# Optimization experiments

Measured on AMD Instinct MI355X. Metric: run time of the kernel, lower is better.

The kernel has to match this reference:

```python
import jax, jax.numpy as jnp
import numpy as np

EMBED_DIM = 1024
NUM_HEADS = 16
HEAD_DIM = EMBED_DIM // NUM_HEADS
LN_EPS = 1e-12
B, S = 2, 2048


def setup_inputs() -> dict:
    key = jax.random.key(0)
    ks = jax.random.split(key, 12)
    scale = 1.0 / np.sqrt(EMBED_DIM)
    d = EMBED_DIM
    return {
        "in_features": jax.random.normal(ks[0], (B, S, d), dtype=jnp.float32),
        "tgt_mask": jnp.ones((B, S), dtype=jnp.float32),
        "Wq": jax.random.normal(ks[1], (d, d), dtype=jnp.float32) * scale,
        "bq": jnp.zeros((d,), dtype=jnp.float32),
        "Wk": jax.random.normal(ks[2], (d, d), dtype=jnp.float32) * scale,
        "bk": jnp.zeros((d,), dtype=jnp.float32),
        "Wv": jax.random.normal(ks[3], (d, d), dtype=jnp.float32) * scale,
        "bv": jnp.zeros((d,), dtype=jnp.float32),
        "Wo": jax.random.normal(ks[4], (d, d), dtype=jnp.float32) * scale,
        "bo": jnp.zeros((d,), dtype=jnp.float32),
        "gamma": jnp.ones((d,), dtype=jnp.float32),
        "beta": jnp.zeros((d,), dtype=jnp.float32),
    }


def _split_heads(x):  # [B,S,D] -> [B,H,S,Dh]
    b, s, _ = x.shape
    return x.reshape(b, s, NUM_HEADS, HEAD_DIM).transpose(0, 2, 1, 3)


def reference(in_features, tgt_mask, Wq, bq, Wk, bk, Wv, bv, Wo, bo, gamma, beta):
    # Self-attention (tgt_features defaults to in_features). Dropout in eval mode (identity).
    q = _split_heads(in_features @ Wq.T + bq)
    k = _split_heads(in_features @ Wk.T + bk)
    v = _split_heads(in_features @ Wv.T + bv)
    # scores: [B,H,S,S]
    scores = jnp.einsum("bhqd,bhkd->bhqk", q, k) / jnp.sqrt(jnp.float32(HEAD_DIM))
    scores = scores + (1.0 - tgt_mask)[:, None, None, :] * (-100000.0)
    attn = jax.nn.softmax(scores, axis=-1)
    ctx = jnp.einsum("bhqk,bhkd->bhqd", attn, v)  # [B,H,S,Dh]
    ctx = ctx.transpose(0, 2, 1, 3).reshape(in_features.shape)  # merge heads
    out = ctx @ Wo.T + bo
    x = out + in_features
    mu = jnp.mean(x, axis=-1, keepdims=True)
    var = jnp.mean(jnp.square(x - mu), axis=-1, keepdims=True)
    return (x - mu) / jnp.sqrt(var + LN_EPS) * gamma + beta
```

## Files before the change

kernel.cpp:

```cpp
#include <hip/hip_runtime.h>
#include <hip/hip_bf16.h>

#define DM   1024
#define HEADS 16
#define DH    64
#define SEQ  2048
#define BATCH   2

typedef __attribute__((ext_vector_type(8))) short short8;
typedef __attribute__((ext_vector_type(4))) short bf16x4;
typedef __attribute__((ext_vector_type(4))) float floatx4;

__device__ __forceinline__ short f2b(float f) {
    union { float f; unsigned u; } v; v.f = f;
    unsigned r = v.u + 0x7FFFu + ((v.u >> 16) & 1u);
    return (short)(r >> 16);
}

__device__ __forceinline__ void async_copy16(const short* gsrc, short* ldst) {
    __builtin_amdgcn_global_load_lds(
        (const __attribute__((address_space(1))) void*)gsrc,
        (__attribute__((address_space(3))) void*)ldst,
        16, 0, 0);
}

__global__ __launch_bounds__(256) void cvt_all(const float* __restrict__ x,
        const float* __restrict__ wq, const float* __restrict__ wk,
        const float* __restrict__ wv, const float* __restrict__ wo,
        short* __restrict__ xb, short* __restrict__ wqkv, short* __restrict__ wob)
{
    const int b = blockIdx.x;
    const float* src; short* dst; int idx;
    if (b < 4096)      { src = x;  dst = xb;                idx = b; }
    else if (b < 5120) { src = wq; dst = wqkv;              idx = b - 4096; }
    else if (b < 6144) { src = wk; dst = wqkv + (1 << 20);  idx = b - 5120; }
    else if (b < 7168) { src = wv; dst = wqkv + (2 << 20);  idx = b - 6144; }
    else               { src = wo; dst = wob;               idx = b - 7168; }
    const int i = idx * 256 + threadIdx.x;
    floatx4 v = ((const floatx4*)src)[i];
    bf16x4 o;
    o.x = f2b(v.x); o.y = f2b(v.y); o.z = f2b(v.z); o.w = f2b(v.w);
    ((bf16x4*)dst)[i] = o;
}

__global__ __launch_bounds__(256) void gemm_qkv(const short* __restrict__ A,
        const short* __restrict__ B,
        const float* __restrict__ bq, const float* __restrict__ bk,
        const float* __restrict__ bv,
        short* __restrict__ qw, short* __restrict__ kw, short* __restrict__ vw)
{
    __shared__ short As[128 * 32];
    __shared__ short Bs[128 * 32];
    const int m0 = blockIdx.x * 128, n0 = blockIdx.y * 128;
    const int w = threadIdx.x >> 6, lane = threadIdx.x & 63;
    const int l16 = lane & 15, quad = lane >> 4;
    const int wm = w >> 1, wn = w & 1;
    const int lr = lane >> 2, lc = (lane & 3) * 8;

    floatx4 acc[4][4];
#pragma unroll
    for (int i = 0; i < 4; ++i)
#pragma unroll
        for (int j = 0; j < 4; ++j) acc[i][j] = (floatx4){0.f, 0.f, 0.f, 0.f};

    for (int kt = 0; kt < DM / 32; ++kt) {
        const int k0 = kt * 32;
        __syncthreads();
        async_copy16(A + (size_t)(m0 + w * 32 + lr) * DM + k0 + lc,      &As[w * 1024]);
        async_copy16(A + (size_t)(m0 + w * 32 + 16 + lr) * DM + k0 + lc, &As[w * 1024 + 512]);
        async_copy16(B + (size_t)(n0 + w * 32 + lr) * DM + k0 + lc,      &Bs[w * 1024]);
        async_copy16(B + (size_t)(n0 + w * 32 + 16 + lr) * DM + k0 + lc, &Bs[w * 1024 + 512]);
        __syncthreads();

        short8 af[4], bf[4];
#pragma unroll
        for (int i = 0; i < 4; ++i)
            af[i] = *(const short8*)&As[(wm * 64 + i * 16 + l16) * 32 + quad * 8];
#pragma unroll
        for (int j = 0; j < 4; ++j)
            bf[j] = *(const short8*)&Bs[(wn * 64 + j * 16 + l16) * 32 + quad * 8];
#pragma unroll
        for (int i = 0; i < 4; ++i)
#pragma unroll
            for (int j = 0; j < 4; ++j)
                acc[i][j] = __builtin_amdgcn_mfma_f32_16x16x32_bf16(af[i], bf[j], acc[i][j], 0, 0, 0);
    }

    const int m_base = m0 + wm * 64 + quad * 4;
#pragma unroll
    for (int j = 0; j < 4; ++j) {
        const int nb = n0 + wn * 64 + j * 16;
        const int t = nb >> 10;
        const int nn = (nb & 1023) + l16;
        const int h = nn >> 6, dh = nn & 63;
        const float* bias = (t == 0) ? bq : (t == 1) ? bk : bv;
        short* dst = (t == 0) ? qw : (t == 1) ? kw : vw;
        const float mulf = (t == 0) ? 0.125f : 1.0f;
        const float bvv = bias[nn];
#pragma unroll
        for (int i = 0; i < 4; ++i)
#pragma unroll
            for (int r = 0; r < 4; ++r) {
                const int m = m_base + i * 16 + r;
                const int b = m >> 11, s = m & (SEQ - 1);
                dst[(((size_t)(b * HEADS + h)) * SEQ + s) * DH + dh] =
                    f2b((acc[i][j][r] + bvv) * mulf);
            }
    }
}

__global__ __launch_bounds__(256) void transpose_v(const short* __restrict__ v,
                                                   short* __restrict__ vt)
{
    __shared__ short tl[64][72];
    const int st = blockIdx.x;
    const int bh = blockIdx.y;
    const int t = threadIdx.x;
    const int row = t >> 2, off = (t & 3) * 16;
    const short* vp = v + ((size_t)bh * SEQ + st * 64 + row) * DH + off;
    *(short8*)&tl[row][off]     = *(const short8*)vp;
    *(short8*)&tl[row][off + 8] = *(const short8*)(vp + 8);
    __syncthreads();
    short8 o0, o1;
#pragma unroll
    for (int j = 0; j < 8; ++j) { o0[j] = tl[off + j][row]; o1[j] = tl[off + 8 + j][row]; }
    short* op = vt + ((size_t)bh * DH + row) * SEQ + st * 64 + off;
    *(short8*)op = o0;
    *(short8*)(op + 8) = o1;
}

__global__ __launch_bounds__(256) void attn_kernel(const short* __restrict__ q,
        const short* __restrict__ k, const short* __restrict__ vt,
        const float* __restrict__ mask, short* __restrict__ ctx)
{
    const int qtile = blockIdx.x;
    const int bh    = blockIdx.y;
    const int bidx  = bh >> 4;
    const int wave = threadIdx.x >> 6, lane = threadIdx.x & 63;
    const int l16 = lane & 15, quad = lane >> 4;
    const int lx = l16 & 7;

    __shared__ short k_lds[64 * 64];
    __shared__ short v_lds[64 * 64];
    __shared__ short p_lds[4][16 * 64];
    __shared__ float madd_lds[SEQ];

    {
        const int t = threadIdx.x;
        const float* mrow = mask + (size_t)bidx * SEQ;
#pragma unroll
        for (int i = 0; i < 8; ++i) {
            const int idx = t * 8 + i;
            madd_lds[idx] = (1.f - mrow[idx]) * (-100000.f);
        }
    }

    const int qrow = qtile * 64 + wave * 16 + l16;
    const short* qbase = q + ((size_t)bh * SEQ + qrow) * DH;
    short8 b_q[2];
#pragma unroll
    for (int ks = 0; ks < 2; ++ks)
        b_q[ks] = *(const short8*)(qbase + ks * 32 + quad * 8);

    float m_own = -1e30f;
    floatx4 o[4];
    floatx4 l_acc = (floatx4){0.f, 0.f, 0.f, 0.f};
#pragma unroll
    for (int d = 0; d < 4; ++d) o[d] = (floatx4){0.f, 0.f, 0.f, 0.f};

    short8 ones;
#pragma unroll
    for (int j = 0; j < 8; ++j) ones[j] = (short)0x3F80;

    const short* kbase0 = k  + (size_t)bh * SEQ * DH;
    const short* vbase0 = vt + (size_t)bh * DH * SEQ;

    for (int kt = 0; kt < SEQ / 64; ++kt) {
        __syncthreads();
        {
            const short* kbase = kbase0 + (size_t)(kt * 64) * DH;
            const short* vbase = vbase0 + kt * 64;
#pragma unroll
            for (int i = 0; i < 2; ++i) {
                const int slot = i * 256 + wave * 64 + lane;
                const int row = slot >> 3, c = slot & 7;
                const int g = c ^ (row & 7);
                async_copy16(kbase + row * DH  + g * 8, &k_lds[(i * 256 + wave * 64) * 8]);
                async_copy16(vbase + (size_t)row * SEQ + g * 8, &v_lds[(i * 256 + wave * 64) * 8]);
            }
        }
        __syncthreads();

        float sv[4][4];
#pragma unroll
        for (int nt = 0; nt < 4; ++nt) {
            floatx4 acc = *(const floatx4*)&madd_lds[kt * 64 + nt * 16 + quad * 4];
#pragma unroll
            for (int ks = 0; ks < 2; ++ks) {
                short8 a = *(const short8*)
                    &k_lds[(nt * 16 + l16) * 64 + (((ks * 4 + quad) ^ lx) * 8)];
                acc = __builtin_amdgcn_mfma_f32_16x16x32_bf16(a, b_q[ks], acc, 0, 0, 0);
            }
#pragma unroll
            for (int r = 0; r < 4; ++r) sv[nt][r] = acc[r];
        }

        float tm = sv[0][0];
#pragma unroll
        for (int nt = 0; nt < 4; ++nt)
#pragma unroll
            for (int r = 0; r < 4; ++r) tm = fmaxf(tm, sv[nt][r]);
        tm = fmaxf(tm, __shfl_xor(tm, 16));
        tm = fmaxf(tm, __shfl_xor(tm, 32));
        const int upd = __any(tm > m_own);
        const float nm = fmaxf(m_own, tm);

#pragma unroll
        for (int nt = 0; nt < 4; ++nt) {
            const float p0 = __expf(sv[nt][0] - nm);
            const float p1 = __expf(sv[nt][1] - nm);
            const float p2 = __expf(sv[nt][2] - nm);
            const float p3 = __expf(sv[nt][3] - nm);
            union { __hip_bfloat162 h[2]; bf16x4 v; } u;
            u.h[0] = __float22bfloat162_rn(make_float2(p0, p1));
            u.h[1] = __float22bfloat162_rn(make_float2(p2, p3));
            *(bf16x4*)&p_lds[wave][l16 * 64 +
                (((nt * 2 + (quad >> 1)) ^ lx) * 8) + (quad & 1) * 4] = u.v;
        }

        if (upd) {
            const float alpha = __expf(m_own - nm);
            float ab[4];
#pragma unroll
            for (int r = 0; r < 4; ++r)
                ab[r] = __shfl(alpha, (lane & 48) | (quad * 4 + r));
#pragma unroll
            for (int d = 0; d < 4; ++d)
#pragma unroll
                for (int r = 0; r < 4; ++r) o[d][r] *= ab[r];
#pragma unroll
            for (int r = 0; r < 4; ++r) l_acc[r] *= ab[r];
        }
        m_own = nm;

#pragma unroll
        for (int ks2 = 0; ks2 < 2; ++ks2) {
            short8 pf = *(const short8*)
                &p_lds[wave][l16 * 64 + (((ks2 * 4 + quad) ^ lx) * 8)];
#pragma unroll
            for (int d = 0; d < 4; ++d) {
                short8 vf = *(const short8*)
                    &v_lds[(d * 16 + l16) * 64 + (((ks2 * 4 + quad) ^ lx) * 8)];
                o[d] = __builtin_amdgcn_mfma_f32_16x16x32_bf16(pf, vf, o[d], 0, 0, 0);
            }
            l_acc = __builtin_amdgcn_mfma_f32_16x16x32_bf16(pf, ones, l_acc, 0, 0, 0);
        }
    }

    const int h = bh & 15, bb = bh >> 4;
    const int srow = qtile * 64 + wave * 16 + quad * 4;
    float rl[4];
#pragma unroll
    for (int r = 0; r < 4; ++r) rl[r] = 1.f / l_acc[r];
#pragma unroll
    for (int d = 0; d < 4; ++d) {
        const int dh = d * 16 + l16;
#pragma unroll
        for (int r = 0; r < 4; ++r) {
            const float val = o[d][r] * rl[r];
            ctx[((size_t)(bb * SEQ + srow + r)) * DM + h * 64 + dh] = f2b(val);
        }
    }
}

__global__ __launch_bounds__(256) void gemm_o(const short* __restrict__ A,
        const short* __restrict__ B, const float* __restrict__ bo,
        const float* __restrict__ xin, float* __restrict__ out)
{
    __shared__ short As[128 * 32];
    __shared__ short Bs[128 * 32];
    const int m0 = blockIdx.x * 128, n0 = blockIdx.y * 128;
    const int w = threadIdx.x >> 6, lane = threadIdx.x & 63;
    const int l16 = lane & 15, quad = lane >> 4;
    const int wm = w >> 1, wn = w & 1;
    const int lr = lane >> 2, lc = (lane & 3) * 8;

    floatx4 acc[4][4];
#pragma unroll
    for (int i = 0; i < 4; ++i)
#pragma unroll
        for (int j = 0; j < 4; ++j) acc[i][j] = (floatx4){0.f, 0.f, 0.f, 0.f};

    for (int kt = 0; kt < DM / 32; ++kt) {
        const int k0 = kt * 32;
        __syncthreads();
        async_copy16(A + (size_t)(m0 + w * 32 + lr) * DM + k0 + lc,      &As[w * 1024]);
        async_copy16(A + (size_t)(m0 + w * 32 + 16 + lr) * DM + k0 + lc, &As[w * 1024 + 512]);
        async_copy16(B + (size_t)(n0 + w * 32 + lr) * DM + k0 + lc,      &Bs[w * 1024]);
        async_copy16(B + (size_t)(n0 + w * 32 + 16 + lr) * DM + k0 + lc, &Bs[w * 1024 + 512]);
        __syncthreads();

        short8 af[4], bf[4];
#pragma unroll
        for (int i = 0; i < 4; ++i)
            af[i] = *(const short8*)&As[(wm * 64 + i * 16 + l16) * 32 + quad * 8];
#pragma unroll
        for (int j = 0; j < 4; ++j)
            bf[j] = *(const short8*)&Bs[(wn * 64 + j * 16 + l16) * 32 + quad * 8];
#pragma unroll
        for (int i = 0; i < 4; ++i)
#pragma unroll
            for (int j = 0; j < 4; ++j)
                acc[i][j] = __builtin_amdgcn_mfma_f32_16x16x32_bf16(af[i], bf[j], acc[i][j], 0, 0, 0);
    }

    const int m_base = m0 + wm * 64 + quad * 4;
#pragma unroll
    for (int j = 0; j < 4; ++j) {
        const int n = n0 + wn * 64 + j * 16 + l16;
        const float bvv = bo[n];
#pragma unroll
        for (int i = 0; i < 4; ++i)
#pragma unroll
            for (int r = 0; r < 4; ++r) {
                const int m = m_base + i * 16 + r;
                const size_t idx = (size_t)m * DM + n;
                out[idx] = acc[i][j][r] + bvv + xin[idx];
            }
    }
}

__global__ __launch_bounds__(256) void ln_kernel(float* __restrict__ y,
        const float* __restrict__ gamma, const float* __restrict__ beta)
{
    const int row = blockIdx.x;
    const int t = threadIdx.x;
    const int wave = t >> 6, lane = t & 63;
    const floatx4 v = ((const floatx4*)(y + (size_t)row * DM))[t];
    float s  = v.x + v.y + v.z + v.w;
    float q2 = v.x * v.x + v.y * v.y + v.z * v.z + v.w * v.w;
#pragma unroll
    for (int off = 1; off < 64; off <<= 1) {
        s  += __shfl_xor(s, off);
        q2 += __shfl_xor(q2, off);
    }
    __shared__ float rs[4], rq[4];
    if (lane == 0) { rs[wave] = s; rq[wave] = q2; }
    __syncthreads();
    const float S  = rs[0] + rs[1] + rs[2] + rs[3];
    const float Q2 = rq[0] + rq[1] + rq[2] + rq[3];
    const float mu = S * (1.f / DM);
    float var = Q2 * (1.f / DM) - mu * mu;
    var = fmaxf(var, 0.f);
    const float rstd = rsqrtf(var + 1e-12f);
    const floatx4 g = ((const floatx4*)gamma)[t];
    const floatx4 bt = ((const floatx4*)beta)[t];
    floatx4 o;
    o.x = (v.x - mu) * rstd * g.x + bt.x;
    o.y = (v.y - mu) * rstd * g.y + bt.y;
    o.z = (v.z - mu) * rstd * g.z + bt.z;
    o.w = (v.w - mu) * rstd * g.w + bt.w;
    ((floatx4*)(y + (size_t)row * DM))[t] = o;
}

extern "C" void kernel_launch(void* const* d_in, const int* in_sizes, int n_in,
                              void* d_out, int out_size, void* d_ws, size_t ws_size,
                              hipStream_t stream) {
    const float* x     = (const float*)d_in[0];
    const float* mask  = (const float*)d_in[1];
    const float* Wq    = (const float*)d_in[2];
    const float* bq    = (const float*)d_in[3];
    const float* Wk    = (const float*)d_in[4];
    const float* bk    = (const float*)d_in[5];
    const float* Wv    = (const float*)d_in[6];
    const float* bv    = (const float*)d_in[7];
    const float* Wo    = (const float*)d_in[8];
    const float* bo    = (const float*)d_in[9];
    const float* gamma = (const float*)d_in[10];
    const float* beta  = (const float*)d_in[11];
    float* out = (float*)d_out;

    const size_t NTOK = (size_t)BATCH * SEQ * DM;
    const size_t WSZ  = (size_t)DM * DM;
    short* xb   = (short*)d_ws;
    short* wqkv = xb + NTOK;
    short* wob  = wqkv + 3 * WSZ;
    short* qw   = wob + WSZ;
    short* kw   = qw + NTOK;
    short* vw   = kw + NTOK;
    short* vtw  = vw + NTOK;
    short* ctxw = vw;

    dim3 blk(256);
    cvt_all<<<dim3(8192), blk, 0, stream>>>(x, Wq, Wk, Wv, Wo, xb, wqkv, wob);
    gemm_qkv<<<dim3(32, 24), blk, 0, stream>>>(xb, wqkv, bq, bk, bv, qw, kw, vw);
    transpose_v<<<dim3(SEQ / 64, BATCH * HEADS), blk, 0, stream>>>(vw, vtw);
    attn_kernel<<<dim3(SEQ / 64, BATCH * HEADS), blk, 0, stream>>>(qw, kw, vtw, mask, ctxw);
    gemm_o<<<dim3(32, 8), blk, 0, stream>>>(ctxw, wob, bo, x, out);
    ln_kernel<<<BATCH * SEQ, blk, 0, stream>>>(out, gamma, beta);
}
```

Baseline: 232.1 us.

## Double-buffer attention K/V loads, fuse V transpose into QKV GEMM, use exp2

The attention kernel now keeps two LDS buffers for K and V, so the next tile's async loads are issued while the current tile is computed. This removes one barrier per iteration. The V transpose kernel is removed: gemm_qkv writes V directly in transposed layout as 4-element packed stores. Q scaling and the additive mask are pre-multiplied by log2(e) so softmax can use exp2, and the mask add is precomputed once in the conversion kernel instead of in every attention block. In exchange the attention kernel uses more LDS and the transposed V stores are strided.

```diff
diff --git a/kernel.cpp b/kernel.cpp
--- a/kernel.cpp
+++ b/kernel.cpp
@@ -6,6 +6,7 @@
 #define DH    64
 #define SEQ  2048
 #define BATCH   2
+#define LOG2E 1.44269504088896f
 
 typedef __attribute__((ext_vector_type(8))) short short8;
 typedef __attribute__((ext_vector_type(4))) short bf16x4;
@@ -16,6 +17,12 @@
     unsigned r = v.u + 0x7FFFu + ((v.u >> 16) & 1u);
     return (short)(r >> 16);
 }
+
+#if __has_builtin(__builtin_amdgcn_exp2f)
+__device__ __forceinline__ float fexp2(float x) { return __builtin_amdgcn_exp2f(x); }
+#else
+__device__ __forceinline__ float fexp2(float x) { return exp2f(x); }
+#endif
 
 __device__ __forceinline__ void async_copy16(const short* gsrc, short* ldst) {
     __builtin_amdgcn_global_load_lds(
@@ -27,9 +34,22 @@
 __global__ __launch_bounds__(256) void cvt_all(const float* __restrict__ x,
         const float* __restrict__ wq, const float* __restrict__ wk,
         const float* __restrict__ wv, const float* __restrict__ wo,
-        short* __restrict__ xb, short* __restrict__ wqkv, short* __restrict__ wob)
+        const float* __restrict__ mask,
+        short* __restrict__ xb, short* __restrict__ wqkv, short* __restrict__ wob,
+        float* __restrict__ maddg)
 {
     const int b = blockIdx.x;
+    if (b >= 8192) {
+        const int bb = b - 8192;
+        const float* mrow = mask + (size_t)bb * SEQ;
+        float* mg = maddg + (size_t)bb * SEQ;
+#pragma unroll
+        for (int i = 0; i < 8; ++i) {
+            const int idx = threadIdx.x * 8 + i;
+            mg[idx] = (1.f - mrow[idx]) * (-100000.f * LOG2E);
+        }
+        return;
+    }
     const float* src; short* dst; int idx;
     if (b < 4096)      { src = x;  dst = xb;                idx = b; }
     else if (b < 5120) { src = wq; dst = wqkv;              idx = b - 4096; }
@@ -47,7 +67,7 @@
         const short* __restrict__ B,
         const float* __restrict__ bq, const float* __restrict__ bk,
         const float* __restrict__ bv,
-        short* __restrict__ qw, short* __restrict__ kw, short* __restrict__ vw)
+        short* __restrict__ qw, short* __restrict__ kw, short* __restrict__ vtw)
 {
     __shared__ short As[128 * 32];
     __shared__ short Bs[128 * 32];
@@ -94,44 +114,38 @@
         const int nn = (nb & 1023) + l16;
         const int h = nn >> 6, dh = nn & 63;
         const float* bias = (t == 0) ? bq : (t == 1) ? bk : bv;
-        short* dst = (t == 0) ? qw : (t == 1) ? kw : vw;
-        const float mulf = (t == 0) ? 0.125f : 1.0f;
         const float bvv = bias[nn];
-#pragma unroll
-        for (int i = 0; i < 4; ++i)
-#pragma unroll
-            for (int r = 0; r < 4; ++r) {
-                const int m = m_base + i * 16 + r;
+        if (t == 2) {
+#pragma unroll
+            for (int i = 0; i < 4; ++i) {
+                const int m = m_base + i * 16;
                 const int b = m >> 11, s = m & (SEQ - 1);
-                dst[(((size_t)(b * HEADS + h)) * SEQ + s) * DH + dh] =
-                    f2b((acc[i][j][r] + bvv) * mulf);
+                bf16x4 p;
+                p.x = f2b(acc[i][j][0] + bvv);
+                p.y = f2b(acc[i][j][1] + bvv);
+                p.z = f2b(acc[i][j][2] + bvv);
+                p.w = f2b(acc[i][j][3] + bvv);
+                *(bf16x4*)&vtw[(((size_t)(b * HEADS + h)) * DH + dh) * SEQ + s] = p;
             }
-    }
-}
-
-__global__ __launch_bounds__(256) void transpose_v(const short* __restrict__ v,
-                                                   short* __restrict__ vt)
-{
-    __shared__ short tl[64][72];
-    const int st = blockIdx.x;
-    const int bh = blockIdx.y;
-    const int t = threadIdx.x;
-    const int row = t >> 2, off = (t & 3) * 16;
-    const short* vp = v + ((size_t)bh * SEQ + st * 64 + row) * DH + off;
-    *(short8*)&tl[row][off]     = *(const short8*)vp;
-    *(short8*)&tl[row][off + 8] = *(const short8*)(vp + 8);
-    __syncthreads();
-    short8 o0, o1;
-#pragma unroll
-    for (int j = 0; j < 8; ++j) { o0[j] = tl[off + j][row]; o1[j] = tl[off + 8 + j][row]; }
-    short* op = vt + ((size_t)bh * DH + row) * SEQ + st * 64 + off;
-    *(short8*)op = o0;
-    *(short8*)(op + 8) = o1;
+        } else {
+            short* dst = (t == 0) ? qw : kw;
+            const float mulf = (t == 0) ? (0.125f * LOG2E) : 1.0f;
+#pragma unroll
+            for (int i = 0; i < 4; ++i)
+#pragma unroll
+                for (int r = 0; r < 4; ++r) {
+                    const int m = m_base + i * 16 + r;
+                    const int b = m >> 11, s = m & (SEQ - 1);
+                    dst[(((size_t)(b * HEADS + h)) * SEQ + s) * DH + dh] =
+                        f2b((acc[i][j][r] + bvv) * mulf);
+                }
+        }
+    }
 }
 
 __global__ __launch_bounds__(256) void attn_kernel(const short* __restrict__ q,
         const short* __restrict__ k, const short* __restrict__ vt,
-        const float* __restrict__ mask, short* __restrict__ ctx)
+        const float* __restrict__ maddg, short* __restrict__ ctx)
 {
     const int qtile = blockIdx.x;
     const int bh    = blockIdx.y;
@@ -140,20 +154,9 @@
     const int l16 = lane & 15, quad = lane >> 4;
     const int lx = l16 & 7;
 
-    __shared__ short k_lds[64 * 64];
-    __shared__ short v_lds[64 * 64];
+    __shared__ short k_lds[2][64 * 64];
+    __shared__ short v_lds[2][64 * 64];
     __shared__ short p_lds[4][16 * 64];
-    __shared__ float madd_lds[SEQ];
-
-    {
-        const int t = threadIdx.x;
-        const float* mrow = mask + (size_t)bidx * SEQ;
-#pragma unroll
-        for (int i = 0; i < 8; ++i) {
-            const int idx = t * 8 + i;
-            madd_lds[idx] = (1.f - mrow[idx]) * (-100000.f);
-        }
-    }
 
     const int qrow = qtile * 64 + wave * 16 + l16;
     const short* qbase = q + ((size_t)bh * SEQ + qrow) * DH;
@@ -174,31 +177,47 @@
 
     const short* kbase0 = k  + (size_t)bh * SEQ * DH;
     const short* vbase0 = vt + (size_t)bh * DH * SEQ;
+    const float* mrow   = maddg + (size_t)bidx * SEQ;
+
+    const int srow0 = (wave * 64 + lane) >> 3;
+    const int srow1 = (256 + wave * 64 + lane) >> 3;
+    const int sc    = lane & 7;
+    const int g0 = sc ^ (srow0 & 7), g1 = sc ^ (srow1 & 7);
+
+    {
+        async_copy16(kbase0 + srow0 * DH + g0 * 8,        &k_lds[0][(wave * 64) * 8]);
+        async_copy16(vbase0 + (size_t)srow0 * SEQ + g0 * 8, &v_lds[0][(wave * 64) * 8]);
+        async_copy16(kbase0 + srow1 * DH + g1 * 8,        &k_lds[0][(256 + wave * 64) * 8]);
+        async_copy16(vbase0 + (size_t)srow1 * SEQ + g1 * 8, &v_lds[0][(256 + wave * 64) * 8]);
+    }
 
     for (int kt = 0; kt < SEQ / 64; ++kt) {
+        const int cur = kt & 1;
         __syncthreads();
-        {
-            const short* kbase = kbase0 + (size_t)(kt * 64) * DH;
-            const short* vbase = vbase0 + kt * 64;
-#pragma unroll
-            for (int i = 0; i < 2; ++i) {
-                const int slot = i * 256 + wave * 64 + lane;
-                const int row = slot >> 3, c = slot & 7;
-                const int g = c ^ (row & 7);
-                async_copy16(kbase + row * DH  + g * 8, &k_lds[(i * 256 + wave * 64) * 8]);
-                async_copy16(vbase + (size_t)row * SEQ + g * 8, &v_lds[(i * 256 + wave * 64) * 8]);
-            }
-        }
-        __syncthreads();
+
+        floatx4 md[4];
+#pragma unroll
+        for (int nt = 0; nt < 4; ++nt)
+            md[nt] = *(const floatx4*)&mrow[kt * 64 + nt * 16 + quad * 4];
+
+        if (kt + 1 < SEQ / 64) {
+            const short* kbase = kbase0 + (size_t)((kt + 1) * 64) * DH;
+            const short* vbase = vbase0 + (kt + 1) * 64;
+            const int nb = 1 - cur;
+            async_copy16(kbase + srow0 * DH + g0 * 8,        &k_lds[nb][(wave * 64) * 8]);
+            async_copy16(vbase + (size_t)srow0 * SEQ + g0 * 8, &v_lds[nb][(wave * 64) * 8]);
+            async_copy16(kbase + srow1 * DH + g1 * 8,        &k_lds[nb][(256 + wave * 64) * 8]);
+            async_copy16(vbase + (size_t)srow1 * SEQ + g1 * 8, &v_lds[nb][(256 + wave * 64) * 8]);
+        }
 
         float sv[4][4];
 #pragma unroll
         for (int nt = 0; nt < 4; ++nt) {
-            floatx4 acc = *(const floatx4*)&madd_lds[kt * 64 + nt * 16 + quad * 4];
+            floatx4 acc = md[nt];
 #pragma unroll
             for (int ks = 0; ks < 2; ++ks) {
                 short8 a = *(const short8*)
-                    &k_lds[(nt * 16 + l16) * 64 + (((ks * 4 + quad) ^ lx) * 8)];
+                    &k_lds[cur][(nt * 16 + l16) * 64 + (((ks * 4 + quad) ^ lx) * 8)];
                 acc = __builtin_amdgcn_mfma_f32_16x16x32_bf16(a, b_q[ks], acc, 0, 0, 0);
             }
 #pragma unroll
@@ -217,10 +236,10 @@
 
 #pragma unroll
         for (int nt = 0; nt < 4; ++nt) {
-            const float p0 = __expf(sv[nt][0] - nm);
-            const float p1 = __expf(sv[nt][1] - nm);
-            const float p2 = __expf(sv[nt][2] - nm);
-            const float p3 = __expf(sv[nt][3] - nm);
+            const float p0 = fexp2(sv[nt][0] - nm);
+            const float p1 = fexp2(sv[nt][1] - nm);
+            const float p2 = fexp2(sv[nt][2] - nm);
+            const float p3 = fexp2(sv[nt][3] - nm);
             union { __hip_bfloat162 h[2]; bf16x4 v; } u;
             u.h[0] = __float22bfloat162_rn(make_float2(p0, p1));
             u.h[1] = __float22bfloat162_rn(make_float2(p2, p3));
@@ -229,7 +248,7 @@
         }
 
         if (upd) {
-            const float alpha = __expf(m_own - nm);
+            const float alpha = fexp2(m_own - nm);
             float ab[4];
 #pragma unroll
             for (int r = 0; r < 4; ++r)
@@ -250,7 +269,7 @@
 #pragma unroll
             for (int d = 0; d < 4; ++d) {
                 short8 vf = *(const short8*)
-                    &v_lds[(d * 16 + l16) * 64 + (((ks2 * 4 + quad) ^ lx) * 8)];
+                    &v_lds[cur][(d * 16 + l16) * 64 + (((ks2 * 4 + quad) ^ lx) * 8)];
                 o[d] = __builtin_amdgcn_mfma_f32_16x16x32_bf16(pf, vf, o[d], 0, 0, 0);
             }
             l_acc = __builtin_amdgcn_mfma_f32_16x16x32_bf16(pf, ones, l_acc, 0, 0, 0);
@@ -387,15 +406,14 @@
     short* wob  = wqkv + 3 * WSZ;
     short* qw   = wob + WSZ;
     short* kw   = qw + NTOK;
-    short* vw   = kw + NTOK;
-    short* vtw  = vw + NTOK;
-    short* ctxw = vw;
+    short* vtw  = kw + NTOK;
+    short* ctxw = vtw + NTOK;
+    float* maddg = (float*)(ctxw + NTOK);
 
     dim3 blk(256);
-    cvt_all<<<dim3(8192), blk, 0, stream>>>(x, Wq, Wk, Wv, Wo, xb, wqkv, wob);
-    gemm_qkv<<<dim3(32, 24), blk, 0, stream>>>(xb, wqkv, bq, bk, bv, qw, kw, vw);
-    transpose_v<<<dim3(SEQ / 64, BATCH * HEADS), blk, 0, stream>>>(vw, vtw);
-    attn_kernel<<<dim3(SEQ / 64, BATCH * HEADS), blk, 0, stream>>>(qw, kw, vtw, mask, ctxw);
+    cvt_all<<<dim3(8194), blk, 0, stream>>>(x, Wq, Wk, Wv, Wo, mask, xb, wqkv, wob, maddg);
+    gemm_qkv<<<dim3(32, 24), blk, 0, stream>>>(xb, wqkv, bq, bk, bv, qw, kw, vtw);
+    attn_kernel<<<dim3(SEQ / 64, BATCH * HEADS), blk, 0, stream>>>(qw, kw, vtw, maddg, ctxw);
     gemm_o<<<dim3(32, 8), blk, 0, stream>>>(ctxw, wob, bo, x, out);
     ln_kernel<<<BATCH * SEQ, blk, 0, stream>>>(out, gamma, beta);
 }
```

After: 241.6 us. +4.1%, slower.

## Use exp2 softmax, precompute mask in global, shrink gemm_o N tile

Applied to the files above, without the earlier changes.

Folds log2(e) into the Q scaling and the mask-add values so the softmax can use a native exp2 instead of __expf. The additive mask is now computed once by the conversion kernel into a global buffer, which drops each attention block's 8 KB LDS mask staging. The mask values are loaded into registers before the barrier so their latency overlaps the K/V copies. Separately, the output projection GEMM tile drops from 128x128 to 128x64, doubling the grid from 256 to 512 blocks to fill more CUs, at the cost of less data reuse per block.

```diff
diff --git a/kernel.cpp b/kernel.cpp
--- a/kernel.cpp
+++ b/kernel.cpp
@@ -6,6 +6,7 @@
 #define DH    64
 #define SEQ  2048
 #define BATCH   2
+#define LOG2E 1.44269504088896f
 
 typedef __attribute__((ext_vector_type(8))) short short8;
 typedef __attribute__((ext_vector_type(4))) short bf16x4;
@@ -16,6 +17,12 @@
     unsigned r = v.u + 0x7FFFu + ((v.u >> 16) & 1u);
     return (short)(r >> 16);
 }
+
+#if __has_builtin(__builtin_amdgcn_exp2f)
+__device__ __forceinline__ float fexp2(float x) { return __builtin_amdgcn_exp2f(x); }
+#else
+__device__ __forceinline__ float fexp2(float x) { return exp2f(x); }
+#endif
 
 __device__ __forceinline__ void async_copy16(const short* gsrc, short* ldst) {
     __builtin_amdgcn_global_load_lds(
@@ -27,9 +34,22 @@
 __global__ __launch_bounds__(256) void cvt_all(const float* __restrict__ x,
         const float* __restrict__ wq, const float* __restrict__ wk,
         const float* __restrict__ wv, const float* __restrict__ wo,
-        short* __restrict__ xb, short* __restrict__ wqkv, short* __restrict__ wob)
+        const float* __restrict__ mask,
+        short* __restrict__ xb, short* __restrict__ wqkv, short* __restrict__ wob,
+        float* __restrict__ maddg)
 {
     const int b = blockIdx.x;
+    if (b >= 8192) {
+        const int bb = b - 8192;
+        const float* mrow = mask + (size_t)bb * SEQ;
+        float* mg = maddg + (size_t)bb * SEQ;
+#pragma unroll
+        for (int i = 0; i < 8; ++i) {
+            const int idx = threadIdx.x * 8 + i;
+            mg[idx] = (1.f - mrow[idx]) * (-100000.f * LOG2E);
+        }
+        return;
+    }
     const float* src; short* dst; int idx;
     if (b < 4096)      { src = x;  dst = xb;                idx = b; }
     else if (b < 5120) { src = wq; dst = wqkv;              idx = b - 4096; }
@@ -95,7 +115,7 @@
         const int h = nn >> 6, dh = nn & 63;
         const float* bias = (t == 0) ? bq : (t == 1) ? bk : bv;
         short* dst = (t == 0) ? qw : (t == 1) ? kw : vw;
-        const float mulf = (t == 0) ? 0.125f : 1.0f;
+        const float mulf = (t == 0) ? (0.125f * LOG2E) : 1.0f;
         const float bvv = bias[nn];
 #pragma unroll
         for (int i = 0; i < 4; ++i)
@@ -131,7 +151,7 @@
 
 __global__ __launch_bounds__(256) void attn_kernel(const short* __restrict__ q,
         const short* __restrict__ k, const short* __restrict__ vt,
-        const float* __restrict__ mask, short* __restrict__ ctx)
+        const float* __restrict__ maddg, short* __restrict__ ctx)
 {
     const int qtile = blockIdx.x;
     const int bh    = blockIdx.y;
@@ -143,17 +163,10 @@
     __shared__ short k_lds[64 * 64];
     __shared__ short v_lds[64 * 64];
     __shared__ short p_lds[4][16 * 64];
-    __shared__ float madd_lds[SEQ];
-
-    {
-        const int t = threadIdx.x;
-        const float* mrow = mask + (size_t)bidx * SEQ;
-#pragma unroll
-        for (int i = 0; i < 8; ++i) {
-            const int idx = t * 8 + i;
-            madd_lds[idx] = (1.f - mrow[idx]) * (-100000.f);
-        }
-    }
+
+    const short* kbase0 = k  + (size_t)bh * SEQ * DH;
+    const short* vbase0 = vt + (size_t)bh * DH * SEQ;
+    const float* mrow   = maddg + (size_t)bidx * SEQ;
 
     const int qrow = qtile * 64 + wave * 16 + l16;
     const short* qbase = q + ((size_t)bh * SEQ + qrow) * DH;
@@ -172,8 +185,13 @@
 #pragma unroll
     for (int j = 0; j < 8; ++j) ones[j] = (short)0x3F80;
 
-    const short* kbase0 = k  + (size_t)bh * SEQ * DH;
-    const short* vbase0 = vt + (size_t)bh * DH * SEQ;
+    int srw[2], gg[2];
+#pragma unroll
+    for (int i = 0; i < 2; ++i) {
+        const int slot = i * 256 + wave * 64 + lane;
+        srw[i] = slot >> 3;
+        gg[i]  = (slot & 7) ^ (srw[i] & 7);
+    }
 
     for (int kt = 0; kt < SEQ / 64; ++kt) {
         __syncthreads();
@@ -182,19 +200,22 @@
             const short* vbase = vbase0 + kt * 64;
 #pragma unroll
             for (int i = 0; i < 2; ++i) {
-                const int slot = i * 256 + wave * 64 + lane;
-                const int row = slot >> 3, c = slot & 7;
-                const int g = c ^ (row & 7);
-                async_copy16(kbase + row * DH  + g * 8, &k_lds[(i * 256 + wave * 64) * 8]);
-                async_copy16(vbase + (size_t)row * SEQ + g * 8, &v_lds[(i * 256 + wave * 64) * 8]);
+                async_copy16(kbase + srw[i] * DH + gg[i] * 8,
+                             &k_lds[(i * 256 + wave * 64) * 8]);
+                async_copy16(vbase + (size_t)srw[i] * SEQ + gg[i] * 8,
+                             &v_lds[(i * 256 + wave * 64) * 8]);
             }
         }
+        floatx4 md[4];
+#pragma unroll
+        for (int nt = 0; nt < 4; ++nt)
+            md[nt] = *(const floatx4*)&mrow[kt * 64 + nt * 16 + quad * 4];
         __syncthreads();
 
         float sv[4][4];
 #pragma unroll
         for (int nt = 0; nt < 4; ++nt) {
-            floatx4 acc = *(const floatx4*)&madd_lds[kt * 64 + nt * 16 + quad * 4];
+            floatx4 acc = md[nt];
 #pragma unroll
             for (int ks = 0; ks < 2; ++ks) {
                 short8 a = *(const short8*)
@@ -217,10 +238,10 @@
 
 #pragma unroll
         for (int nt = 0; nt < 4; ++nt) {
-            const float p0 = __expf(sv[nt][0] - nm);
-            const float p1 = __expf(sv[nt][1] - nm);
-            const float p2 = __expf(sv[nt][2] - nm);
-            const float p3 = __expf(sv[nt][3] - nm);
+            const float p0 = fexp2(sv[nt][0] - nm);
+            const float p1 = fexp2(sv[nt][1] - nm);
+            const float p2 = fexp2(sv[nt][2] - nm);
+            const float p3 = fexp2(sv[nt][3] - nm);
             union { __hip_bfloat162 h[2]; bf16x4 v; } u;
             u.h[0] = __float22bfloat162_rn(make_float2(p0, p1));
             u.h[1] = __float22bfloat162_rn(make_float2(p2, p3));
@@ -229,7 +250,7 @@
         }
 
         if (upd) {
-            const float alpha = __expf(m_own - nm);
+            const float alpha = fexp2(m_own - nm);
             float ab[4];
 #pragma unroll
             for (int r = 0; r < 4; ++r)
@@ -278,46 +299,51 @@
         const float* __restrict__ xin, float* __restrict__ out)
 {
     __shared__ short As[128 * 32];
-    __shared__ short Bs[128 * 32];
-    const int m0 = blockIdx.x * 128, n0 = blockIdx.y * 128;
+    __shared__ short Bs[64 * 32];
+    const int m0 = blockIdx.x * 128, n0 = blockIdx.y * 64;
     const int w = threadIdx.x >> 6, lane = threadIdx.x & 63;
     const int l16 = lane & 15, quad = lane >> 4;
     const int wm = w >> 1, wn = w & 1;
-    const int lr = lane >> 2, lc = (lane & 3) * 8;
-
-    floatx4 acc[4][4];
+
+    floatx4 acc[4][2];
 #pragma unroll
     for (int i = 0; i < 4; ++i)
 #pragma unroll
-        for (int j = 0; j < 4; ++j) acc[i][j] = (floatx4){0.f, 0.f, 0.f, 0.f};
+        for (int j = 0; j < 2; ++j) acc[i][j] = (floatx4){0.f, 0.f, 0.f, 0.f};
+
+    const int c0 = w * 64 + lane;
 
     for (int kt = 0; kt < DM / 32; ++kt) {
         const int k0 = kt * 32;
         __syncthreads();
-        async_copy16(A + (size_t)(m0 + w * 32 + lr) * DM + k0 + lc,      &As[w * 1024]);
-        async_copy16(A + (size_t)(m0 + w * 32 + 16 + lr) * DM + k0 + lc, &As[w * 1024 + 512]);
-        async_copy16(B + (size_t)(n0 + w * 32 + lr) * DM + k0 + lc,      &Bs[w * 1024]);
-        async_copy16(B + (size_t)(n0 + w * 32 + 16 + lr) * DM + k0 + lc, &Bs[w * 1024 + 512]);
-        __syncthreads();
-
-        short8 af[4], bf[4];
+        {
+            const int ra0 = c0 >> 2,          ca0 = (c0 & 3) * 8;
+            const int ra1 = (256 + c0) >> 2,  ca1 = (c0 & 3) * 8;
+            async_copy16(A + (size_t)(m0 + ra0) * DM + k0 + ca0, &As[(w * 64) * 8]);
+            async_copy16(A + (size_t)(m0 + ra1) * DM + k0 + ca1, &As[(256 + w * 64) * 8]);
+            const int rb = c0 >> 2, cb = (c0 & 3) * 8;
+            async_copy16(B + (size_t)(n0 + rb) * DM + k0 + cb,   &Bs[(w * 64) * 8]);
+        }
+        __syncthreads();
+
+        short8 af[4], bf[2];
 #pragma unroll
         for (int i = 0; i < 4; ++i)
             af[i] = *(const short8*)&As[(wm * 64 + i * 16 + l16) * 32 + quad * 8];
 #pragma unroll
-        for (int j = 0; j < 4; ++j)
-            bf[j] = *(const short8*)&Bs[(wn * 64 + j * 16 + l16) * 32 + quad * 8];
-#pragma unroll
-        for (int i = 0; i < 4; ++i)
-#pragma unroll
-            for (int j = 0; j < 4; ++j)
+        for (int j = 0; j < 2; ++j)
+            bf[j] = *(const short8*)&Bs[(wn * 32 + j * 16 + l16) * 32 + quad * 8];
+#pragma unroll
+        for (int i = 0; i < 4; ++i)
+#pragma unroll
+            for (int j = 0; j < 2; ++j)
                 acc[i][j] = __builtin_amdgcn_mfma_f32_16x16x32_bf16(af[i], bf[j], acc[i][j], 0, 0, 0);
     }
 
     const int m_base = m0 + wm * 64 + quad * 4;
 #pragma unroll
-    for (int j = 0; j < 4; ++j) {
-        const int n = n0 + wn * 64 + j * 16 + l16;
+    for (int j = 0; j < 2; ++j) {
+        const int n = n0 + wn * 32 + j * 16 + l16;
         const float bvv = bo[n];
 #pragma unroll
         for (int i = 0; i < 4; ++i)
@@ -390,12 +416,13 @@
     short* vw   = kw + NTOK;
     short* vtw  = vw + NTOK;
     short* ctxw = vw;
+    float* maddg = (float*)(vtw + NTOK);
 
     dim3 blk(256);
-    cvt_all<<<dim3(8192), blk, 0, stream>>>(x, Wq, Wk, Wv, Wo, xb, wqkv, wob);
+    cvt_all<<<dim3(8194), blk, 0, stream>>>(x, Wq, Wk, Wv, Wo, mask, xb, wqkv, wob, maddg);
     gemm_qkv<<<dim3(32, 24), blk, 0, stream>>>(xb, wqkv, bq, bk, bv, qw, kw, vw);
     transpose_v<<<dim3(SEQ / 64, BATCH * HEADS), blk, 0, stream>>>(vw, vtw);
-    attn_kernel<<<dim3(SEQ / 64, BATCH * HEADS), blk, 0, stream>>>(qw, kw, vtw, mask, ctxw);
-    gemm_o<<<dim3(32, 8), blk, 0, stream>>>(ctxw, wob, bo, x, out);
+    attn_kernel<<<dim3(SEQ / 64, BATCH * HEADS), blk, 0, stream>>>(qw, kw, vtw, maddg, ctxw);
+    gemm_o<<<dim3(32, 16), blk, 0, stream>>>(ctxw, wob, bo, x, out);
     ln_kernel<<<BATCH * SEQ, blk, 0, stream>>>(out, gamma, beta);
 }
```

New measurement: 230.4 us. Within noise of the previous version (-0.7%).
